# Kernel tuning notes

Hardware: AMD Instinct MI355X
Metric: run time of the kernel (lower is better)

Reference implementation:

```python
import jax, jax.numpy as jnp
import numpy as np

EMBED_DIM = 1024
NUM_HEADS = 16
HEAD_DIM = EMBED_DIM // NUM_HEADS
ROPE_BASE = 10000.0
NEG_INF = -1e9


def _rope_tables(T, dim, dtype=jnp.float32):
    inv_freq = 1.0 / (ROPE_BASE ** (jnp.arange(0, dim, 2, dtype=jnp.float32) / dim))
    t = jnp.arange(T, dtype=jnp.float32)
    freqs = jnp.einsum('t,f->tf', t, inv_freq)          # [T, dim/2]
    emb = jnp.concatenate([freqs, freqs], axis=-1)       # [T, dim]
    return jnp.cos(emb).astype(dtype), jnp.sin(emb).astype(dtype)


def _rotate_half(x):
    x1, x2 = jnp.split(x, 2, axis=-1)
    return jnp.concatenate([-x2, x1], axis=-1)


def setup_inputs() -> dict:
    key = jax.random.key(0)
    kx, kqkv, kout = jax.random.split(key, 3)
    B, T = 2, 2048
    x = jax.random.normal(kx, (B, T, EMBED_DIM), dtype=jnp.float32)
    # Dense kernels (no bias), glorot-ish scale
    w_qkv = jax.random.normal(kqkv, (EMBED_DIM, 3 * EMBED_DIM), dtype=jnp.float32) * (EMBED_DIM ** -0.5)
    w_out = jax.random.normal(kout, (EMBED_DIM, EMBED_DIM), dtype=jnp.float32) * (EMBED_DIM ** -0.5)
    return {"x": x, "w_qkv": w_qkv, "w_out": w_out}


def reference(x, w_qkv, w_out):
    B, T, _ = x.shape
    qkv = x @ w_qkv                                      # [B, T, 3E]
    q, k, v = jnp.split(qkv, 3, axis=-1)

    def split_heads(t):
        return t.reshape(B, T, NUM_HEADS, HEAD_DIM).transpose(0, 2, 1, 3)  # [B,H,T,D]

    q, k, v = split_heads(q), split_heads(k), split_heads(v)

    cos, sin = _rope_tables(T, HEAD_DIM, x.dtype)        # [T, D]
    cos = cos[None, None, :, :]
    sin = sin[None, None, :, :]
    q = q * cos + _rotate_half(q) * sin
    k = k * cos + _rotate_half(k) * sin

    scale = jnp.sqrt(jnp.asarray(HEAD_DIM, dtype=jnp.float32)).astype(x.dtype)
    scores = jnp.einsum('bhqd,bhkd->bhqk', q, k) / scale  # [B,H,T,T]
    causal = jnp.tril(jnp.ones((T, T), dtype=bool))[None, None, :, :]
    scores = jnp.where(causal, scores, jnp.asarray(NEG_INF, dtype=x.dtype))
    probs = jax.nn.softmax(scores, axis=-1)
    out = jnp.einsum('bhqk,bhkd->bhqd', probs, v)         # [B,H,T,D]
    out = out.transpose(0, 2, 1, 3).reshape(B, T, EMBED_DIM)
    return out @ w_out
```

## Files before the change

kernel.cpp:

```cpp
#include <hip/hip_runtime.h>
#include <hip/hip_bf16.h>
#include <cstdint>

#define DI __device__ __forceinline__

using u16x8  = __attribute__((ext_vector_type(8))) unsigned short;
using u32x4  = __attribute__((ext_vector_type(4))) unsigned int;
using bf16x8 = __attribute__((ext_vector_type(8))) __bf16;
using f32x4  = __attribute__((ext_vector_type(4))) float;


DI unsigned short f2bf(float f) {
  unsigned u = __builtin_bit_cast(unsigned, f);
  u += 0x7fffu + ((u >> 16) & 1u);
  return (unsigned short)(u >> 16);
}
DI float bf2f(unsigned short b) {
  unsigned u = (unsigned)b << 16;
  return __builtin_bit_cast(float, u);
}
DI unsigned cvt_pk_bf16(float lo, float hi) {
  unsigned r;
  asm("v_cvt_pk_bf16_f32 %0, %1, %2" : "=v"(r) : "v"(lo), "v"(hi));
  return r;
}
DI void permlane_swap32(unsigned& a, unsigned& b) {
  asm("v_permlane32_swap_b32 %0, %1" : "+v"(a), "+v"(b));
}
DI void permlane_swap16(unsigned& a, unsigned& b) {
  asm("v_permlane16_swap_b32 %0, %1" : "+v"(a), "+v"(b));
}

DI void gld_lds16(const void* g, void* l) {
  __builtin_amdgcn_global_load_lds(
      (const __attribute__((address_space(1))) void*)(uintptr_t)g,
      (__attribute__((address_space(3))) void*)(uint32_t)(uintptr_t)l,
      16, 0, 0);
}

DI void wait_vm8() { asm volatile("s_waitcnt vmcnt(8)" ::: "memory"); }
DI void wait_vm4() { asm volatile("s_waitcnt vmcnt(4)" ::: "memory"); }
DI void wait_vm0() { asm volatile("s_waitcnt vmcnt(0)" ::: "memory"); }
DI void sched_fence() { asm volatile("" ::: "memory"); }


__global__ __launch_bounds__(256) void cvt_bf16_kernel(const float* __restrict__ in,
                                                        unsigned short* __restrict__ out, int n) {
  int i = (blockIdx.x * 256 + threadIdx.x) * 8;
  if (i >= n) return;
  float4 v0 = *(const float4*)(in + i);
  float4 v1 = *(const float4*)(in + i + 4);
  u16x8 o;
  o[0] = f2bf(v0.x); o[1] = f2bf(v0.y); o[2] = f2bf(v0.z); o[3] = f2bf(v0.w);
  o[4] = f2bf(v1.x); o[5] = f2bf(v1.y); o[6] = f2bf(v1.z); o[7] = f2bf(v1.w);
  *(u16x8*)(out + i) = o;
}

__global__ __launch_bounds__(256) void transpose_cvt_kernel(const float* __restrict__ in,
                                                             unsigned short* __restrict__ out,
                                                             int K, int N) {
  __shared__ float tile[32][33];
  int n0 = blockIdx.x * 32, k0 = blockIdx.y * 32;
  int tx = threadIdx.x & 31, ty = threadIdx.x >> 5;
#pragma unroll
  for (int i = 0; i < 4; ++i)
    tile[ty * 4 + i][tx] = in[(size_t)(k0 + ty * 4 + i) * N + n0 + tx];
  __syncthreads();
#pragma unroll
  for (int i = 0; i < 4; ++i)
    out[(size_t)(n0 + ty * 4 + i) * K + k0 + tx] = f2bf(tile[tx][ty * 4 + i]);
}


template <int MT>
DI void rope_rows(const f32x4 (&acc)[8][4], unsigned short* __restrict__ dst,
                  int gm0, int h, float qs, int r15, int g4) {
#pragma unroll
  for (int r = 0; r < 4; ++r) {
    int mrow = gm0 + MT * 16 + g4 * 4 + r;
    int b = mrow >> 11, t = mrow & 2047;
    unsigned short* rowp = dst + (((size_t)(b * 16 + h) * 2048 + t) << 6);
    float tf = (float)t;
#pragma unroll
    for (int nt = 0; nt < 2; ++nt) {
      int j = nt * 16 + r15;
      float invf = exp2f((float)j * -0.4152410118609203f);
      float ang = tf * invf;
      float sv, cv;
      sincosf(ang, &sv, &cv);
      float x1 = acc[MT][nt][r], x2 = acc[MT][nt + 2][r];
      rowp[j]      = f2bf((x1 * cv - x2 * sv) * qs);
      rowp[j + 32] = f2bf((x2 * cv + x1 * sv) * qs);
    }
  }
}

template <int P>
DI void vtrans_pass(const f32x4 (&acc)[8][4], short* __restrict__ tb,
                    unsigned short* __restrict__ vhead, int t0, int lane, int r15, int g4) {
#pragma unroll
  for (int np = 0; np < 2; ++np)
#pragma unroll
    for (int mt = 0; mt < 8; ++mt)
#pragma unroll
      for (int pr = 0; pr < 2; ++pr) {
        unsigned pk = cvt_pk_bf16(acc[mt][2 * P + np][2 * pr], acc[mt][2 * P + np][2 * pr + 1]);
        *(unsigned*)(tb + (np * 16 + r15) * 136 + mt * 16 + g4 * 4 + pr * 2) = pk;
      }
#pragma unroll
  for (int cc = 0; cc < 8; ++cc) {
    int dl = (cc & 3) * 8 + (lane >> 3);
    int tc = (lane & 7) * 8 + (cc >> 2) * 64;
    u16x8 vv = *(const u16x8*)(tb + dl * 136 + tc);
    *(u16x8*)(vhead + (size_t)(P * 32 + dl) * 2048 + t0 + tc) = vv;
  }
}


__global__ __launch_bounds__(512, 2)
void gemm256_qkv(const unsigned short* __restrict__ A, const unsigned short* __restrict__ B,
                 unsigned short* __restrict__ q_out, unsigned short* __restrict__ k_out,
                 unsigned short* __restrict__ v_out, int M, int N, int K) {
  __shared__ __align__(16) char smem[4][32768];
  const int tid = threadIdx.x;
  const int lane = tid & 63, wave = tid >> 6;
  const int wr = wave >> 2, wc = wave & 3;
  const int r15 = lane & 15, g4 = lane >> 4;

  const int id = blockIdx.x;
  const int g = (id & 7) * 24 + (id >> 3);
  const int by = g / 12, bx = g % 12;
  const int m0 = by << 8, n0 = bx << 8;

  const size_t Ks = (size_t)K;
  const unsigned short* aptr = A + (size_t)(m0 + wave * 32 + r15) * Ks + g4 * 8;
  const unsigned short* bptr = B + (size_t)(n0 + wave * 32 + r15) * Ks + g4 * 8;

  f32x4 acc[8][4] = {};
  const int NT = K >> 5;

  auto stage = [&](int slot, int tt) {
    const unsigned short* ak = aptr + tt * 32;
    const unsigned short* bk = bptr + tt * 32;
    char* sA = &smem[slot][0]     + wave * 2048;
    char* sB = &smem[slot][16384] + wave * 2048;
    gld_lds16(ak,           sA);
    gld_lds16(ak + 16 * Ks, sA + 1024);
    gld_lds16(bk,           sB);
    gld_lds16(bk + 16 * Ks, sB + 1024);
  };

  auto body = [&](int t) {
    sched_fence();
    const char* sA = &smem[t & 3][0];
    const char* sB = &smem[t & 3][16384];
    bf16x8 af[8], bfr[4];
#pragma unroll
    for (int mt = 0; mt < 8; ++mt)
      af[mt] = *(const bf16x8*)(sA + (wr * 8 + mt) * 1024 + lane * 16);
#pragma unroll
    for (int nt = 0; nt < 4; ++nt)
      bfr[nt] = *(const bf16x8*)(sB + (wc * 4 + nt) * 1024 + lane * 16);
    if (t + 3 < NT) stage((t + 3) & 3, t + 3);
    __builtin_amdgcn_s_setprio(1);
#pragma unroll
    for (int mt = 0; mt < 8; ++mt)
#pragma unroll
      for (int nt = 0; nt < 4; ++nt)
        acc[mt][nt] = __builtin_amdgcn_mfma_f32_16x16x32_bf16(af[mt], bfr[nt], acc[mt][nt], 0, 0, 0);
    __builtin_amdgcn_s_setprio(0);
  };

  stage(0, 0); stage(1, 1); stage(2, 2);
  for (int t = 0; t < NT - 2; ++t) {
    wait_vm8();
    __builtin_amdgcn_s_barrier();
    body(t);
  }
  wait_vm4();
  __builtin_amdgcn_s_barrier();
  body(NT - 2);
  wait_vm0();
  __builtin_amdgcn_s_barrier();
  body(NT - 1);

  __syncthreads();

  const int gm0 = m0 + wr * 128, gn0 = n0 + wc * 64;
  const int region = gn0 >> 10;
  const int h = (gn0 & 1023) >> 6;
  if (region <= 1) {
    unsigned short* dst = (region == 0) ? q_out : k_out;
    const float qs = (region == 0) ? (0.125f * 1.44269504088896341f) : 1.0f;
    rope_rows<0>(acc, dst, gm0, h, qs, r15, g4);
    rope_rows<1>(acc, dst, gm0, h, qs, r15, g4);
    rope_rows<2>(acc, dst, gm0, h, qs, r15, g4);
    rope_rows<3>(acc, dst, gm0, h, qs, r15, g4);
    rope_rows<4>(acc, dst, gm0, h, qs, r15, g4);
    rope_rows<5>(acc, dst, gm0, h, qs, r15, g4);
    rope_rows<6>(acc, dst, gm0, h, qs, r15, g4);
    rope_rows<7>(acc, dst, gm0, h, qs, r15, g4);
  } else {
    const int b = gm0 >> 11, t0 = gm0 & 2047;
    unsigned short* vhead = v_out + ((size_t)(b * 16 + h) * 64) * 2048;
    short* tb = (short*)(&smem[0][0] + wave * 16384);
    vtrans_pass<0>(acc, tb, vhead, t0, lane, r15, g4);
    vtrans_pass<1>(acc, tb, vhead, t0, lane, r15, g4);
  }
}


__global__ __launch_bounds__(256, 2)
void gemm_proj(const unsigned short* __restrict__ A, const unsigned short* __restrict__ B,
               float* __restrict__ c_out, int M, int N, int K) {
  __shared__ __align__(16) char smem[4][16384];
  const int tid = threadIdx.x;
  const int lane = tid & 63, wave = tid >> 6;
  const int wm = wave >> 1, wn = wave & 1;
  const int r15 = lane & 15, g4 = lane >> 4;

  const int id = blockIdx.x;
  const int xcd = id & 7, rr = id >> 3;
  const int m0 = rr << 7, n0 = xcd << 7;

  const size_t Ks = (size_t)K;
  const unsigned short* aptr = A + (size_t)(m0 + wave * 32 + r15) * Ks + g4 * 8;
  const unsigned short* bptr = B + (size_t)(n0 + wave * 32 + r15) * Ks + g4 * 8;

  f32x4 acc[4][4] = {};
  const int NT = K >> 5;

  auto stage = [&](int slot, int tt) {
    const unsigned short* ak = aptr + tt * 32;
    const unsigned short* bk = bptr + tt * 32;
    char* sA = &smem[slot][0]    + wave * 2048;
    char* sB = &smem[slot][8192] + wave * 2048;
    gld_lds16(ak,           sA);
    gld_lds16(ak + 16 * Ks, sA + 1024);
    gld_lds16(bk,           sB);
    gld_lds16(bk + 16 * Ks, sB + 1024);
  };

  auto body = [&](int t) {
    sched_fence();
    const char* sA = &smem[t & 3][0];
    const char* sB = &smem[t & 3][8192];
    bf16x8 af[4], bfr[4];
#pragma unroll
    for (int mt = 0; mt < 4; ++mt)
      af[mt] = *(const bf16x8*)(sA + (wm * 4 + mt) * 1024 + lane * 16);
#pragma unroll
    for (int nt = 0; nt < 4; ++nt)
      bfr[nt] = *(const bf16x8*)(sB + (wn * 4 + nt) * 1024 + lane * 16);
    if (t + 3 < NT) stage((t + 3) & 3, t + 3);
    __builtin_amdgcn_s_setprio(1);
#pragma unroll
    for (int mt = 0; mt < 4; ++mt)
#pragma unroll
      for (int nt = 0; nt < 4; ++nt)
        acc[mt][nt] = __builtin_amdgcn_mfma_f32_16x16x32_bf16(af[mt], bfr[nt], acc[mt][nt], 0, 0, 0);
    __builtin_amdgcn_s_setprio(0);
  };

  stage(0, 0); stage(1, 1); stage(2, 2);
  for (int t = 0; t < NT - 2; ++t) {
    wait_vm8();
    __builtin_amdgcn_s_barrier();
    body(t);
  }
  wait_vm4();
  __builtin_amdgcn_s_barrier();
  body(NT - 2);
  wait_vm0();
  __builtin_amdgcn_s_barrier();
  body(NT - 1);

  const int gm0 = m0 + wm * 64, gn0 = n0 + wn * 64;
#pragma unroll
  for (int mt = 0; mt < 4; ++mt)
#pragma unroll
    for (int r = 0; r < 4; ++r) {
      int mrow = gm0 + mt * 16 + g4 * 4 + r;
      float* rowp = c_out + (size_t)mrow * N + gn0;
#pragma unroll
      for (int nt = 0; nt < 4; ++nt)
        rowp[nt * 16 + r15] = acc[mt][nt][r];
    }
}


__device__ const int RBMAP[24] = {7, 23, 20, 21, 18, 19, 17, 5,
                                  22, 6, 16, 12, 13, 14, 15, 10,
                                  0, 1, 2, 3, 8, 9, 4, 11};

__global__ __launch_bounds__(256)
void attn_fused(const unsigned short* __restrict__ qb, const unsigned short* __restrict__ kb,
                const unsigned short* __restrict__ vt, unsigned short* __restrict__ attno,
                unsigned short* __restrict__ pO, float* __restrict__ pml) {
  __shared__ __align__(16) char ksm[3][8192];
  __shared__ __align__(16) char vsm[3][8192];

  const int tid = threadIdx.x, lane = tid & 63, wave = tid >> 6;
  const int r15 = lane & 15, g4 = lane >> 4;

  const int wg = blockIdx.x;
  const int qq = wg >> 3;
  const int bh = (wg & 7) * 4 + qq / 24;
  const int rb = RBMAP[qq % 24];
  int J, c; bool multi;
  if (rb < 8) { J = rb; c = 0; multi = false; }
  else { int rr = rb - 8; J = 8 + (rr >> 1); c = rr & 1; multi = true; }
  const int ntw = 2 * J + 2;
  const int ktmid = J + 1;
  const int kt0 = (multi && c) ? ktmid : 0;
  const int ktN = multi ? (c ? ntw : ktmid) : ntw;
  const int NTW = ktN - kt0;
  const int q0 = J << 7;
  const int q0w = q0 + wave * 32;

  const size_t hb = (size_t)bh * 2048 * 64;
  const unsigned short* Qp = qb + hb;
  const unsigned short* Kp = kb + hb;
  const unsigned short* Vp = vt + hb;

  bf16x8 qf[2][2];
#pragma unroll
  for (int mq = 0; mq < 2; ++mq)
#pragma unroll
    for (int kc = 0; kc < 2; ++kc)
      qf[mq][kc] = *(const bf16x8*)(Qp + (size_t)(q0w + mq * 16 + r15) * 64 + kc * 32 + g4 * 8);

  f32x4 o[2][4] = {};
  float mr[2] = {-INFINITY, -INFINITY};
  float lr[2] = {0.f, 0.f};

  auto stage = [&](int slot, int kt) {
    const int kv0 = kt << 6;
#pragma unroll
    for (int i = 0; i < 2; ++i) {
      int f = wave * 2 + i;
      int nt = f >> 1, kc = f & 1;
      gld_lds16(Kp + (size_t)(kv0 + nt * 16 + r15) * 64 + kc * 32 + g4 * 8, &ksm[slot][f * 1024]);
      gld_lds16(Vp + (size_t)(nt * 16 + r15) * 2048 + kv0 + kc * 32 + g4 * 8, &vsm[slot][f * 1024]);
    }
  };

  auto process = [&](int slot, int kv0, bool mask) {
    bf16x8 kf[8];
#pragma unroll
    for (int i = 0; i < 8; ++i)
      kf[i] = *(const bf16x8*)(&ksm[slot][i * 1024] + lane * 16);

    f32x4 s[4][2] = {};
    __builtin_amdgcn_s_setprio(1);
#pragma unroll
    for (int nt = 0; nt < 4; ++nt)
#pragma unroll
      for (int kc = 0; kc < 2; ++kc) {
        s[nt][0] = __builtin_amdgcn_mfma_f32_16x16x32_bf16(kf[nt * 2 + kc], qf[0][kc], s[nt][0], 0, 0, 0);
        s[nt][1] = __builtin_amdgcn_mfma_f32_16x16x32_bf16(kf[nt * 2 + kc], qf[1][kc], s[nt][1], 0, 0, 0);
      }
    __builtin_amdgcn_s_setprio(0);

    if (mask) {
#pragma unroll
      for (int nt = 0; nt < 4; ++nt)
#pragma unroll
        for (int mq = 0; mq < 2; ++mq)
#pragma unroll
          for (int r = 0; r < 4; ++r)
            if (kv0 + nt * 16 + g4 * 4 + r > q0w + mq * 16 + r15) s[nt][mq][r] = -1e9f;
    }

    bf16x8 pa[2][2];
#pragma unroll
    for (int mq = 0; mq < 2; ++mq) {
      float m0 = fmaxf(fmaxf(s[0][mq][0], s[0][mq][1]), fmaxf(s[0][mq][2], s[0][mq][3]));
      float m1 = fmaxf(fmaxf(s[1][mq][0], s[1][mq][1]), fmaxf(s[1][mq][2], s[1][mq][3]));
      float m2 = fmaxf(fmaxf(s[2][mq][0], s[2][mq][1]), fmaxf(s[2][mq][2], s[2][mq][3]));
      float m3 = fmaxf(fmaxf(s[3][mq][0], s[3][mq][1]), fmaxf(s[3][mq][2], s[3][mq][3]));
      float mx = fmaxf(fmaxf(m0, m1), fmaxf(m2, m3));
      mx = fmaxf(mx, __shfl_xor(mx, 16));
      mx = fmaxf(mx, __shfl_xor(mx, 32));
      float mnew;
      if (!__all(mx <= mr[mq] + 8.f)) {
        mnew = fmaxf(mr[mq], mx);
        float fsc = exp2f(mr[mq] - mnew);
        mr[mq] = mnew;
        lr[mq] *= fsc;
#pragma unroll
        for (int r = 0; r < 4; ++r) {
          float fr = __shfl(fsc, (g4 << 2) + r);
#pragma unroll
          for (int dt = 0; dt < 4; ++dt) o[mq][dt][r] *= fr;
        }
      } else {
        mnew = mr[mq];
      }
      float t0 = 0.f, t1 = 0.f, t2 = 0.f, t3 = 0.f;
#pragma unroll
      for (int nt = 0; nt < 4; ++nt) {
        float p0 = exp2f(s[nt][mq][0] - mnew);
        float p1 = exp2f(s[nt][mq][1] - mnew);
        float p2 = exp2f(s[nt][mq][2] - mnew);
        float p3 = exp2f(s[nt][mq][3] - mnew);
        s[nt][mq][0] = p0; s[nt][mq][1] = p1; s[nt][mq][2] = p2; s[nt][mq][3] = p3;
        if (nt == 0) t0 = (p0 + p1) + (p2 + p3);
        if (nt == 1) t1 = (p0 + p1) + (p2 + p3);
        if (nt == 2) t2 = (p0 + p1) + (p2 + p3);
        if (nt == 3) t3 = (p0 + p1) + (p2 + p3);
      }
      float ps = (t0 + t1) + (t2 + t3);
      ps += __shfl_xor(ps, 16);
      ps += __shfl_xor(ps, 32);
      lr[mq] += ps;
      unsigned p32[4][2];
#pragma unroll
      for (int nt = 0; nt < 4; ++nt) {
        p32[nt][0] = cvt_pk_bf16(s[nt][mq][0], s[nt][mq][1]);
        p32[nt][1] = cvt_pk_bf16(s[nt][mq][2], s[nt][mq][3]);
      }
#pragma unroll
      for (int kc = 0; kc < 2; ++kc) {
        u32x4 w;
#pragma unroll
        for (int pi = 0; pi < 2; ++pi) {
          unsigned a = p32[2 * kc][pi], b = p32[2 * kc + 1][pi];
          permlane_swap32(a, b);
          permlane_swap16(a, b);
          w[pi] = a;
          w[2 + pi] = b;
        }
        pa[mq][kc] = __builtin_bit_cast(bf16x8, w);
      }
    }

    bf16x8 vf[8];
#pragma unroll
    for (int i = 0; i < 8; ++i)
      vf[i] = *(const bf16x8*)(&vsm[slot][i * 1024] + lane * 16);

    __builtin_amdgcn_s_setprio(1);
#pragma unroll
    for (int kc = 0; kc < 2; ++kc)
#pragma unroll
      for (int dt = 0; dt < 4; ++dt) {
        o[0][dt] = __builtin_amdgcn_mfma_f32_16x16x32_bf16(pa[0][kc], vf[dt * 2 + kc], o[0][dt], 0, 0, 0);
        o[1][dt] = __builtin_amdgcn_mfma_f32_16x16x32_bf16(pa[1][kc], vf[dt * 2 + kc], o[1][dt], 0, 0, 0);
      }
    __builtin_amdgcn_s_setprio(0);
  };

  stage(0, kt0);
  if (NTW > 1) stage(1, kt0 + 1);
  for (int i = 0; i < NTW; ++i) {
    if (i + 1 < NTW) wait_vm4(); else wait_vm0();
    __builtin_amdgcn_s_barrier();
    sched_fence();
    if (i + 2 < NTW) stage((i + 2) % 3, kt0 + i + 2);
    const int kv0 = (kt0 + i) << 6;
    if (kv0 <= q0w + 31)
      process(i % 3, kv0, kv0 + 63 > q0w);
  }

  if (!multi) {
    const int b = bh >> 4, h = bh & 15;
#pragma unroll
    for (int mq = 0; mq < 2; ++mq) {
      float inv = 1.f / lr[mq];
#pragma unroll
      for (int r = 0; r < 4; ++r) {
        float ir = __shfl(inv, (g4 << 2) + r);
        int q = q0w + mq * 16 + g4 * 4 + r;
        unsigned short* rowp = attno + (size_t)(b * 2048 + q) * 1024 + h * 64;
#pragma unroll
        for (int dt = 0; dt < 4; ++dt)
          rowp[dt * 16 + r15] = f2bf(o[mq][dt][r] * ir);
      }
    }
  } else {
    const int sidx = (bh * 8 + (J - 8)) * 2 + c;
    unsigned short* po = pO + (size_t)sidx * 8192 + wave * 32 * 64;
#pragma unroll
    for (int mq = 0; mq < 2; ++mq)
#pragma unroll
      for (int r = 0; r < 4; ++r)
#pragma unroll
        for (int dt = 0; dt < 4; ++dt)
          po[(mq * 16 + g4 * 4 + r) * 64 + dt * 16 + r15] = f2bf(o[mq][dt][r]);
    if (g4 == 0) {
      float* pm = pml + sidx * 256 + wave * 32;
#pragma unroll
      for (int mq = 0; mq < 2; ++mq) {
        pm[mq * 16 + r15] = mr[mq];
        pm[128 + mq * 16 + r15] = lr[mq];
      }
    }
  }
}

__global__ __launch_bounds__(256)
void attn_combine(const unsigned short* __restrict__ pO, const float* __restrict__ pml,
                  unsigned short* __restrict__ attno) {
  const int bx = blockIdx.x;
  const int bh = bx >> 3, Jrel = bx & 7, J = 8 + Jrel;
  const int t = threadIdx.x;
  const int row = t >> 1;
  const int dh = (t & 1) << 5;
  const int s0i = (bh * 8 + Jrel) * 2;
  const float* pm0 = pml + s0i * 256;
  const float* pm1 = pm0 + 256;
  float m0 = pm0[row], l0 = pm0[128 + row];
  float m1 = pm1[row], l1 = pm1[128 + row];
  float mg = fmaxf(m0, m1);
  float s0 = exp2f(m0 - mg), s1 = exp2f(m1 - mg);
  float inv = 1.f / (l0 * s0 + l1 * s1);
  s0 *= inv; s1 *= inv;
  const unsigned short* o0 = pO + (size_t)s0i * 8192 + row * 64 + dh;
  const unsigned short* o1 = o0 + 8192;
  const int b = bh >> 4, h = bh & 15;
  const int q = J * 128 + row;
  unsigned short* dst = attno + (size_t)(b * 2048 + q) * 1024 + h * 64 + dh;
#pragma unroll
  for (int dd = 0; dd < 32; dd += 8) {
    u16x8 a = *(const u16x8*)(o0 + dd);
    u16x8 bq = *(const u16x8*)(o1 + dd);
    u16x8 ov;
#pragma unroll
    for (int e = 0; e < 8; ++e)
      ov[e] = f2bf(bf2f(a[e]) * s0 + bf2f(bq[e]) * s1);
    *(u16x8*)(dst + dd) = ov;
  }
}


extern "C" void kernel_launch(void* const* d_in, const int* in_sizes, int n_in,
                              void* d_out, int out_size, void* d_ws, size_t ws_size,
                              hipStream_t stream) {
  const float* x     = (const float*)d_in[0];
  const float* w_qkv = (const float*)d_in[1];
  const float* w_out = (const float*)d_in[2];
  float* out = (float*)d_out;

  char* ws = (char*)d_ws;
  unsigned short* xb  = (unsigned short*)(ws);
  unsigned short* wqT = (unsigned short*)(ws + (8u << 20));
  unsigned short* woT = (unsigned short*)(ws + (14u << 20));
  unsigned short* qb  = (unsigned short*)(ws + (16u << 20));
  unsigned short* kb  = (unsigned short*)(ws + (24u << 20));
  unsigned short* vt  = (unsigned short*)(ws + (32u << 20));
  unsigned short* ao  = (unsigned short*)(ws + (40u << 20));
  unsigned short* pO  = xb;
  float*          pml = (float*)wqT;

  cvt_bf16_kernel<<<2048, 256, 0, stream>>>(x, xb, 4096 * 1024);
  transpose_cvt_kernel<<<dim3(96, 32), 256, 0, stream>>>(w_qkv, wqT, 1024, 3072);
  transpose_cvt_kernel<<<dim3(32, 32), 256, 0, stream>>>(w_out, woT, 1024, 1024);
  gemm256_qkv<<<192, 512, 0, stream>>>(xb, wqT, qb, kb, vt, 4096, 3072, 1024);
  attn_fused<<<768, 256, 0, stream>>>(qb, kb, vt, ao, pO, pml);
  attn_combine<<<256, 256, 0, stream>>>(pO, pml, ao);
  gemm_proj<<<256, 256, 0, stream>>>(ao, woT, out, 4096, 1024, 1024);
}
```

Before: 144.7 us.

## Split causal attention rows into up to four KV chunks for finer load balance

Query row-blocks are now split across 1-4 KV chunks depending on their causal length, giving 1280 workgroups instead of 768, with a new 40-entry scheduling map ordering the longest work first. The combine kernel merges up to four partial outputs using their stored max and sum statistics. Partial outputs go into the output buffer and the xb buffer, both free at that point, to fit the larger partial storage. This is meant to even out per-workgroup work and fill the GPU's compute units better, at the cost of more partial writes and a heavier combine pass.

```diff
diff --git a/kernel.cpp b/kernel.cpp
--- a/kernel.cpp
+++ b/kernel.cpp
@@ -289,14 +289,24 @@
 }
 
 
-__device__ const int RBMAP[24] = {7, 23, 20, 21, 18, 19, 17, 5,
-                                  22, 6, 16, 12, 13, 14, 15, 10,
-                                  0, 1, 2, 3, 8, 9, 4, 11};
+__device__ const int RBMAP40[40] = {
+  3, 10, 11, 20, 21, 22, 23, 33, 35, 36, 37, 38, 39,
+  8, 9, 16, 17, 18, 19, 25, 27, 28, 29, 30, 31, 32, 34,
+  2, 6, 7, 12, 13, 14, 15, 24, 26,
+  4, 5,
+  1,
+  0
+};
+
+DI unsigned short* part_ptr(unsigned short* p0, unsigned short* p1, int sidx) {
+  return (sidx < 1024) ? p0 + (size_t)sidx * 8192 : p1 + (size_t)(sidx - 1024) * 8192;
+}
 
 __global__ __launch_bounds__(256)
 void attn_fused(const unsigned short* __restrict__ qb, const unsigned short* __restrict__ kb,
                 const unsigned short* __restrict__ vt, unsigned short* __restrict__ attno,
-                unsigned short* __restrict__ pO, float* __restrict__ pml) {
+                unsigned short* __restrict__ pO0, unsigned short* __restrict__ pO1,
+                float* __restrict__ pml) {
   __shared__ __align__(16) char ksm[3][8192];
   __shared__ __align__(16) char vsm[3][8192];
 
@@ -304,19 +314,20 @@
   const int r15 = lane & 15, g4 = lane >> 4;
 
   const int wg = blockIdx.x;
-  const int qq = wg >> 3;
-  const int bh = (wg & 7) * 4 + qq / 24;
-  const int rb = RBMAP[qq % 24];
-  int J, c; bool multi;
-  if (rb < 8) { J = rb; c = 0; multi = false; }
-  else { int rr = rb - 8; J = 8 + (rr >> 1); c = rr & 1; multi = true; }
-  const int ntw = 2 * J + 2;
-  const int ktmid = J + 1;
-  const int kt0 = (multi && c) ? ktmid : 0;
-  const int ktN = multi ? (c ? ntw : ktmid) : ntw;
+  const int swz = (wg & 7) * 160 + (wg >> 3);
+  const int bh = swz / 40;
+  const int rb = RBMAP40[swz % 40];
+  int J, c, nc;
+  if (rb < 4)       { J = rb;                 c = 0;            nc = 1; }
+  else if (rb < 12) { J = 4 + ((rb - 4) >> 1);  c = (rb - 4) & 1;  nc = 2; }
+  else if (rb < 24) { int r = rb - 12; J = 8 + r / 3;  c = r % 3;  nc = 3; }
+  else              { int r = rb - 24; J = 12 + (r >> 2); c = r & 3; nc = 4; }
+  const int T = 2 * J + 2;
+  const int kt0 = (c * T) / nc;
+  const int ktN = ((c + 1) * T) / nc;
   const int NTW = ktN - kt0;
-  const int q0 = J << 7;
-  const int q0w = q0 + wave * 32;
+  const bool multi = (nc > 1);
+  const int q0w = (J << 7) + wave * 32;
 
   const size_t hb = (size_t)bh * 2048 * 64;
   const unsigned short* Qp = qb + hb;
@@ -479,8 +490,11 @@
       }
     }
   } else {
-    const int sidx = (bh * 8 + (J - 8)) * 2 + c;
-    unsigned short* po = pO + (size_t)sidx * 8192 + wave * 32 * 64;
+    const int slot = (J < 8) ? (J - 4) * 2 + c
+                   : (J < 12) ? 8 + (J - 8) * 3 + c
+                              : 20 + (J - 12) * 4 + c;
+    const int sidx = bh * 36 + slot;
+    unsigned short* po = part_ptr(pO0, pO1, sidx) + wave * 32 * 64;
 #pragma unroll
     for (int mq = 0; mq < 2; ++mq)
 #pragma unroll
@@ -500,35 +514,60 @@
 }
 
 __global__ __launch_bounds__(256)
-void attn_combine(const unsigned short* __restrict__ pO, const float* __restrict__ pml,
-                  unsigned short* __restrict__ attno) {
+void attn_combine(unsigned short* __restrict__ pO0, unsigned short* __restrict__ pO1,
+                  const float* __restrict__ pml, unsigned short* __restrict__ attno) {
   const int bx = blockIdx.x;
-  const int bh = bx >> 3, Jrel = bx & 7, J = 8 + Jrel;
+  const int bh = bx / 12, jj = bx % 12, J = 4 + jj;
+  const int nc = (jj < 4) ? 2 : (jj < 8) ? 3 : 4;
+  const int slotbase = (jj < 4) ? jj * 2 : (jj < 8) ? 8 + (jj - 4) * 3 : 20 + (jj - 8) * 4;
   const int t = threadIdx.x;
   const int row = t >> 1;
   const int dh = (t & 1) << 5;
-  const int s0i = (bh * 8 + Jrel) * 2;
-  const float* pm0 = pml + s0i * 256;
-  const float* pm1 = pm0 + 256;
-  float m0 = pm0[row], l0 = pm0[128 + row];
-  float m1 = pm1[row], l1 = pm1[128 + row];
-  float mg = fmaxf(m0, m1);
-  float s0 = exp2f(m0 - mg), s1 = exp2f(m1 - mg);
-  float inv = 1.f / (l0 * s0 + l1 * s1);
-  s0 *= inv; s1 *= inv;
-  const unsigned short* o0 = pO + (size_t)s0i * 8192 + row * 64 + dh;
-  const unsigned short* o1 = o0 + 8192;
+
+  float mv[4], lv[4];
+  float mg = -INFINITY;
+#pragma unroll
+  for (int cc = 0; cc < 4; ++cc)
+    if (cc < nc) {
+      const int sidx = bh * 36 + slotbase + cc;
+      mv[cc] = pml[sidx * 256 + row];
+      lv[cc] = pml[sidx * 256 + 128 + row];
+      mg = fmaxf(mg, mv[cc]);
+    }
+  float denom = 0.f;
+#pragma unroll
+  for (int cc = 0; cc < 4; ++cc)
+    if (cc < nc) {
+      mv[cc] = exp2f(mv[cc] - mg);
+      denom += lv[cc] * mv[cc];
+    }
+  const float inv = 1.f / denom;
+
+  float av[32] = {};
+#pragma unroll
+  for (int cc = 0; cc < 4; ++cc)
+    if (cc < nc) {
+      const int sidx = bh * 36 + slotbase + cc;
+      const unsigned short* op = part_ptr(pO0, pO1, sidx) + row * 64 + dh;
+      const float w = mv[cc] * inv;
+#pragma unroll
+      for (int dd = 0; dd < 32; dd += 8) {
+        u16x8 a = *(const u16x8*)(op + dd);
+#pragma unroll
+        for (int e = 0; e < 8; ++e)
+          av[dd + e] += bf2f(a[e]) * w;
+      }
+    }
+
   const int b = bh >> 4, h = bh & 15;
   const int q = J * 128 + row;
   unsigned short* dst = attno + (size_t)(b * 2048 + q) * 1024 + h * 64 + dh;
 #pragma unroll
   for (int dd = 0; dd < 32; dd += 8) {
-    u16x8 a = *(const u16x8*)(o0 + dd);
-    u16x8 bq = *(const u16x8*)(o1 + dd);
     u16x8 ov;
 #pragma unroll
     for (int e = 0; e < 8; ++e)
-      ov[e] = f2bf(bf2f(a[e]) * s0 + bf2f(bq[e]) * s1);
+      ov[e] = f2bf(av[dd + e]);
     *(u16x8*)(dst + dd) = ov;
   }
 }
@@ -550,14 +589,15 @@
   unsigned short* kb  = (unsigned short*)(ws + (24u << 20));
   unsigned short* vt  = (unsigned short*)(ws + (32u << 20));
   unsigned short* ao  = (unsigned short*)(ws + (40u << 20));
-  unsigned short* pO  = xb;
+  unsigned short* pO0 = (unsigned short*)d_out;
+  unsigned short* pO1 = xb;
   float*          pml = (float*)wqT;
 
   cvt_bf16_kernel<<<2048, 256, 0, stream>>>(x, xb, 4096 * 1024);
   transpose_cvt_kernel<<<dim3(96, 32), 256, 0, stream>>>(w_qkv, wqT, 1024, 3072);
   transpose_cvt_kernel<<<dim3(32, 32), 256, 0, stream>>>(w_out, woT, 1024, 1024);
   gemm256_qkv<<<192, 512, 0, stream>>>(xb, wqT, qb, kb, vt, 4096, 3072, 1024);
-  attn_fused<<<768, 256, 0, stream>>>(qb, kb, vt, ao, pO, pml);
-  attn_combine<<<256, 256, 0, stream>>>(pO, pml, ao);
+  attn_fused<<<1280, 256, 0, stream>>>(qb, kb, vt, ao, pO0, pO1, pml);
+  attn_combine<<<384, 256, 0, stream>>>(pO0, pO1, pml, ao);
   gemm_proj<<<256, 256, 0, stream>>>(ao, woT, out, 4096, 1024, 1024);
 }
```

New measurement: 142.1 us. About the same (-1.8%).
